# Performance work log

Hardware: AMD Instinct MI355X
Metric: run time of the kernel (lower is better)

## Reference

```python
import jax, jax.numpy as jnp
import numpy as np

HIDDEN = 2048
NUM_HEADS = 16
HEAD_DIM = HIDDEN // NUM_HEADS  # 128
ROPE_BASE = 10000.0


def setup_inputs() -> dict:
    key = jax.random.key(0)
    ks = jax.random.split(key, 5)
    B, T, C = 2, 2048, HIDDEN
    scale = 1.0 / np.sqrt(C)
    x = jax.random.normal(ks[0], (B, T, C), dtype=jnp.float32)
    Wq = jax.random.normal(ks[1], (C, C), dtype=jnp.float32) * scale
    Wk = jax.random.normal(ks[2], (C, C), dtype=jnp.float32) * scale
    Wv = jax.random.normal(ks[3], (C, C), dtype=jnp.float32) * scale
    Wo = jax.random.normal(ks[4], (C, C), dtype=jnp.float32) * scale
    return {"x": x, "Wq": Wq, "Wk": Wk, "Wv": Wv, "Wo": Wo}


def _rope_cos_sin(T, dtype):
    # inv_freq: [D/2]; emb: [T, D] = cat(freqs, freqs)
    inv_freq = 1.0 / (ROPE_BASE ** (jnp.arange(0, HEAD_DIM, 2, dtype=jnp.float32) / HEAD_DIM))
    t = jnp.arange(T, dtype=jnp.float32)
    freqs = t[:, None] * inv_freq[None, :]          # [T, D/2]
    emb = jnp.concatenate([freqs, freqs], axis=-1)  # [T, D]
    # broadcast shape [1, T, 1, D] to match q/k [B, T, H, D]
    return jnp.cos(emb)[None, :, None, :].astype(dtype), jnp.sin(emb)[None, :, None, :].astype(dtype)


def _rotate_half(u):
    u1, u2 = jnp.split(u, 2, axis=-1)
    return jnp.concatenate([-u2, u1], axis=-1)


def reference(x, Wq, Wk, Wv, Wo):
    B, T, C = x.shape
    H, D = NUM_HEADS, HEAD_DIM
    # QKV projections (torch Linear: x @ W.T). Weights here stored as [C, C] so use x @ W.
    q = (x @ Wq).reshape(B, T, H, D)
    k = (x @ Wk).reshape(B, T, H, D)
    v = (x @ Wv).reshape(B, T, H, D)
    cos, sin = _rope_cos_sin(T, x.dtype)
    q = q * cos + _rotate_half(q) * sin
    k = k * cos + _rotate_half(k) * sin
    # causal SDPA: scores [B, H, T, T]
    scale = 1.0 / jnp.sqrt(jnp.asarray(D, dtype=x.dtype))
    scores = jnp.einsum('bqhd,bkhd->bhqk', q, k) * scale
    causal = jnp.tril(jnp.ones((T, T), dtype=bool))
    scores = jnp.where(causal[None, None, :, :], scores, jnp.asarray(-jnp.inf, dtype=scores.dtype))
    attn = jax.nn.softmax(scores, axis=-1)
    out = jnp.einsum('bhqk,bkhd->bqhd', attn, v).reshape(B, T, C)
    return out @ Wo
```

## Files before the change

### kernel.cpp

```cpp
#include <hip/hip_runtime.h>
#include <hip/hip_bf16.h>

#define C_DIM 2048
#define NHEAD 16
#define HD 128
#define BB 2
#define TT 2048
#define MM (BB * TT)
#define NQT 32
#define N3 (3 * C_DIM)

typedef short short4v __attribute__((ext_vector_type(4)));
typedef short short8v __attribute__((ext_vector_type(8)));
typedef __bf16 bf16x4 __attribute__((ext_vector_type(4)));
typedef __bf16 bf16x8 __attribute__((ext_vector_type(8)));
typedef float f32x4 __attribute__((ext_vector_type(4)));

#define AS1 __attribute__((address_space(1)))
#define AS3 __attribute__((address_space(3)))

#define VMCNT(n) asm volatile("s_waitcnt vmcnt(" #n ")" ::: "memory")

__device__ __forceinline__ void load_lds16(const void* g, void* l) {
  __builtin_amdgcn_global_load_lds((const AS1 void*)g, (AS3 void*)l, 16, 0, 0);
}

__device__ __forceinline__ short f2bf(float f) {
  union { float f; unsigned u; } v; v.f = f;
  unsigned u = v.u;
  u += 0x7FFFu + ((u >> 16) & 1u);
  return (short)(u >> 16);
}
__device__ __forceinline__ float bf2f(short s) {
  union { unsigned u; float f; } v;
  v.u = ((unsigned)(unsigned short)s) << 16;
  return v.f;
}

__device__ __forceinline__ float exp2_fast(float x) {
  float r;
  asm("v_exp_f32 %0, %1" : "=v"(r) : "v"(x));
  return r;
}

__global__ __launch_bounds__(256) void cvt_x(const float* __restrict__ in,
                                             short* __restrict__ out, int n4) {
  int i = blockIdx.x * 256 + threadIdx.x;
  int stride = gridDim.x * 256;
  for (int idx = i; idx < n4; idx += stride) {
    float4 f = ((const float4*)in)[idx];
    short4v o;
    o[0] = f2bf(f.x); o[1] = f2bf(f.y); o[2] = f2bf(f.z); o[3] = f2bf(f.w);
    ((short4v*)out)[idx] = o;
  }
}

__global__ __launch_bounds__(256) void cvt_w_t(const float* __restrict__ W,
                                               short* __restrict__ Wt) {
  __shared__ float tile[32][33];
  int bx = blockIdx.x;
  int by = blockIdx.y;
  int lx = threadIdx.x & 31;
  int ly = threadIdx.x >> 5;
#pragma unroll
  for (int j = 0; j < 4; ++j) {
    int r = by * 32 + ly + j * 8;
    tile[ly + j * 8][lx] = W[(size_t)r * C_DIM + bx * 32 + lx];
  }
  __syncthreads();
#pragma unroll
  for (int j = 0; j < 4; ++j) {
    int n = bx * 32 + ly + j * 8;
    Wt[(size_t)n * C_DIM + by * 32 + lx] = f2bf(tile[lx][ly + j * 8]);
  }
}

__global__ __launch_bounds__(256) void rope_tab(float2* __restrict__ tab) {
  int idx = blockIdx.x * 256 + threadIdx.x;
  int t = idx >> 6, d = idx & 63;
  float inv = expf(-9.210340371976184f * (float)d * (1.0f / 64.0f));
  float a = (float)t * inv;
  tab[idx] = make_float2(cosf(a), sinf(a));
}

template <bool F32OUT>
__global__ __launch_bounds__(256, 2) void gemm8p(const short* __restrict__ A,
                                                 const short* __restrict__ Bt,
                                                 void* __restrict__ Cout,
                                                 int M, int N, int K, int NBN) {
  __shared__ short sA[2][128 * 64];
  __shared__ short sB[2][128 * 64];
  const int tid = threadIdx.x;
  const int lane = tid & 63;
  const int w = tid >> 6;
  const int wm = w >> 1, wn = w & 1;
  const int r = lane & 15, g = lane >> 4;

  const int wg = blockIdx.x;
  const int mb = wg / NBN, nb = wg % NBN;
  const int m0 = mb * 128, n0 = nb * 128;

  f32x4 acc[4][4] = {};

  auto stage = [&](int buf, int kt) {
#pragma unroll
    for (int j = 0; j < 4; ++j) {
      int p = j * 256 + tid;
      int row = p >> 3;
      int c16 = (p & 7) ^ (row & 7);
      load_lds16(A + (size_t)(m0 + row) * K + kt * 64 + c16 * 8,
                 &sA[buf][(j * 256 + w * 64) * 8]);
    }
#pragma unroll
    for (int j = 0; j < 4; ++j) {
      int p = j * 256 + tid;
      int row = p >> 3;
      int c16 = (p & 7) ^ (row & 7);
      load_lds16(Bt + (size_t)(n0 + row) * K + kt * 64 + c16 * 8,
                 &sB[buf][(j * 256 + w * 64) * 8]);
    }
  };

  auto compute = [&](int buf) {
#pragma unroll
    for (int kk = 0; kk < 2; ++kk) {
      bf16x8 af[4], bv[4];
#pragma unroll
      for (int m = 0; m < 4; ++m) {
        int row = wm * 64 + m * 16 + r;
        af[m] = *(const bf16x8*)((const char*)&sA[buf][0] + row * 128 +
                                 (((kk * 4 + g) ^ (row & 7)) << 4));
      }
#pragma unroll
      for (int n = 0; n < 4; ++n) {
        int row = wn * 64 + n * 16 + r;
        bv[n] = *(const bf16x8*)((const char*)&sB[buf][0] + row * 128 +
                                 (((kk * 4 + g) ^ (row & 7)) << 4));
      }
      __builtin_amdgcn_s_setprio(1);
#pragma unroll
      for (int m = 0; m < 4; ++m)
#pragma unroll
        for (int n = 0; n < 4; ++n)
          acc[m][n] = __builtin_amdgcn_mfma_f32_16x16x32_bf16(af[m], bv[n], acc[m][n], 0, 0, 0);
      __builtin_amdgcn_s_setprio(0);
    }
  };

  const int NT = K >> 6;
  stage(0, 0);
  stage(1, 1);
  VMCNT(8);
  __builtin_amdgcn_s_barrier();

  for (int t = 0; t < NT; ++t) {
    const int cur = t & 1;
    compute(cur);
    if (t + 1 < NT) {
      asm volatile("" ::: "memory");
      __builtin_amdgcn_s_barrier();
      if (t + 2 < NT) {
        stage(cur, t + 2);
        VMCNT(8);
      } else {
        VMCNT(0);
      }
      asm volatile("" ::: "memory");
      __builtin_amdgcn_s_barrier();
    }
  }

#pragma unroll
  for (int m = 0; m < 4; ++m)
#pragma unroll
    for (int n = 0; n < 4; ++n)
#pragma unroll
      for (int q = 0; q < 4; ++q) {
        int row = m0 + wm * 64 + m * 16 + g * 4 + q;
        int col = n0 + wn * 64 + n * 16 + r;
        size_t off = (size_t)row * N + col;
        if constexpr (F32OUT) ((float*)Cout)[off] = acc[m][n][q];
        else ((short*)Cout)[off] = f2bf(acc[m][n][q]);
      }
}

__global__ __launch_bounds__(256) void rope_qk(const short* __restrict__ qkv,
                                               const float2* __restrict__ tab,
                                               short* __restrict__ Qr,
                                               short* __restrict__ Kr) {
  const short* src = qkv + (blockIdx.y ? C_DIM : 0);
  short* dst = blockIdx.y ? Kr : Qr;
  const float qs = blockIdx.y ? 1.0f : 0.12751744f;
  int rid = blockIdx.x * 4 + (threadIdx.x >> 6);
  int lane = threadIdx.x & 63;
  int t = rid & (TT - 1);
  int bh = rid >> 11;
  int b = bh >> 4, h = bh & 15;
  const short* in = src + ((size_t)(b * TT + t)) * N3 + h * HD;
  float f0 = bf2f(in[lane]);
  float f1 = bf2f(in[lane + 64]);
  float2 cs = tab[t * 64 + lane];
  dst[(size_t)rid * HD + lane]      = f2bf((f0 * cs.x - f1 * cs.y) * qs);
  dst[(size_t)rid * HD + lane + 64] = f2bf((f1 * cs.x + f0 * cs.y) * qs);
}

__global__ __launch_bounds__(256) void v_tr(const short* __restrict__ qkv,
                                            short* __restrict__ Vt) {
  __shared__ short tl[64][132];
  int bh = blockIdx.y, b = bh >> 4, h = bh & 15;
  int t0 = blockIdx.x * 64;
  int tid = threadIdx.x;
  const short* vsrc = qkv + 2 * C_DIM;
#pragma unroll
  for (int i = 0; i < 4; ++i) {
    int c = i * 256 + tid;
    int row = c >> 4, cc = c & 15;
    short8v v = *(const short8v*)(vsrc + ((size_t)(b * TT + t0 + row)) * N3 + h * HD + cc * 8);
#pragma unroll
    for (int j = 0; j < 8; ++j) tl[row][cc * 8 + j] = v[j];
  }
  __syncthreads();
  int d = tid >> 1, half = tid & 1;
#pragma unroll
  for (int u = 0; u < 4; ++u) {
    short8v ov;
#pragma unroll
    for (int j = 0; j < 8; ++j) ov[j] = tl[half * 32 + u * 8 + j][d];
    *(short8v*)(Vt + ((size_t)bh * HD + d) * TT + t0 + half * 32 + u * 8) = ov;
  }
}

__global__ __launch_bounds__(256) void attn_dual(const short* __restrict__ Qr,
                                                 const short* __restrict__ Kr,
                                                 const short* __restrict__ Vt,
                                                 short* __restrict__ AO) {
  const int qa = blockIdx.x;
  const int qb = NQT - 1 - qa;
  const int bh = blockIdx.y;
  const int b = bh >> 4, h = bh & 15;
  const int tid = threadIdx.x;
  const int lane = tid & 63;
  const int w = tid >> 6;
  const int r = lane & 15, g = lane >> 4;

  __shared__ short sK[64 * 128];
  __shared__ short sV[128 * 64];
  __shared__ short sPa[4][16 * 72];
  __shared__ short sPb[4][16 * 72];

  auto loadQ = [&](bf16x8* qf, int q0) {
    const short* qbp = Qr + ((size_t)bh * TT + q0 + w * 16 + r) * HD + g * 8;
#pragma unroll
    for (int s = 0; s < 4; ++s) qf[s] = *(const bf16x8*)(qbp + s * 32);
  };

  bf16x8 qfA[4], qfB[4];
  loadQ(qfA, qa * 64);
  loadQ(qfB, qb * 64);

  f32x4 oA[8] = {}, oB[8] = {};
  float mA = -1e30f, mB = -1e30f;
  float lA = 0.f, lB = 0.f;

  short8v kreg[4], vreg[4];
  auto stage_load = [&](int kt) {
#pragma unroll
    for (int i = 0; i < 4; ++i) {
      int c = i * 256 + tid;
      kreg[i] = *(const short8v*)(Kr + ((size_t)bh * TT + kt * 64 + (c >> 4)) * HD + (c & 15) * 8);
    }
#pragma unroll
    for (int i = 0; i < 4; ++i) {
      int c = i * 256 + tid;
      vreg[i] = *(const short8v*)(Vt + ((size_t)bh * HD + (c >> 3)) * TT + kt * 64 + (c & 7) * 8);
    }
  };
  auto stage_write = [&]() {
#pragma unroll
    for (int i = 0; i < 4; ++i) {
      int c = i * 256 + tid;
      int row = c >> 4, cc = c & 15;
      int addr = (row * 256 + cc * 16) ^ ((row & 7) << 4);
      *(short8v*)((char*)sK + addr) = kreg[i];
    }
#pragma unroll
    for (int i = 0; i < 4; ++i) {
      int c = i * 256 + tid;
      int row = c >> 3, cc = c & 7;
      int addr = (row * 128 + cc * 16) ^ ((row & 7) << 4);
      *(short8v*)((char*)sV + addr) = vreg[i];
    }
  };

  auto process = [&](const bf16x8* qf, f32x4* o, float& m, float& l, bool diag,
                     short* pw) {
    f32x4 sacc[4] = {};
    __builtin_amdgcn_s_setprio(1);
#pragma unroll
    for (int nf = 0; nf < 4; ++nf) {
#pragma unroll
      for (int ss = 0; ss < 4; ++ss) {
        int krow = nf * 16 + r;
        int addr = (krow * 256 + (ss * 32 + g * 8) * 2) ^ ((krow & 7) << 4);
        bf16x8 kf = *(const bf16x8*)((char*)sK + addr);
        sacc[nf] = __builtin_amdgcn_mfma_f32_16x16x32_bf16(kf, qf[ss], sacc[nf], 0, 0, 0);
      }
    }
    __builtin_amdgcn_s_setprio(0);

    if (diag) {
#pragma unroll
      for (int nf = 0; nf < 4; ++nf)
#pragma unroll
        for (int q = 0; q < 4; ++q)
          if (nf * 16 + g * 4 + q > w * 16 + r) sacc[nf][q] = -1e30f;
    }

    float p01 = fmaxf(fmaxf(sacc[0][0], sacc[0][1]), fmaxf(sacc[0][2], sacc[0][3]));
    float p23 = fmaxf(fmaxf(sacc[1][0], sacc[1][1]), fmaxf(sacc[1][2], sacc[1][3]));
    float p45 = fmaxf(fmaxf(sacc[2][0], sacc[2][1]), fmaxf(sacc[2][2], sacc[2][3]));
    float p67 = fmaxf(fmaxf(sacc[3][0], sacc[3][1]), fmaxf(sacc[3][2], sacc[3][3]));
    float pmax = fmaxf(fmaxf(p01, p23), fmaxf(p45, p67));
    pmax = fmaxf(pmax, __shfl_xor(pmax, 16, 64));
    pmax = fmaxf(pmax, __shfl_xor(pmax, 32, 64));

    if (!__all(pmax - m <= 8.0f)) {
      float mnew = fmaxf(m, pmax);
      float alpha = exp2_fast(m - mnew);
      m = mnew;
      l *= alpha;
#pragma unroll
      for (int q = 0; q < 4; ++q) {
        float aq = __shfl(alpha, (g * 4 + q) | (lane & 48), 64);
#pragma unroll
        for (int nf2 = 0; nf2 < 8; ++nf2) o[nf2][q] *= aq;
      }
    }

    float s16 = 0.f;
#pragma unroll
    for (int nf = 0; nf < 4; ++nf) {
      f32x4 pe;
#pragma unroll
      for (int q = 0; q < 4; ++q) pe[q] = exp2_fast(sacc[nf][q] - m);
      s16 += (pe[0] + pe[1]) + (pe[2] + pe[3]);
      *(bf16x4*)(pw + r * 72 + nf * 16 + g * 4) = __builtin_convertvector(pe, bf16x4);
    }
    float rs = s16;
    rs += __shfl_xor(rs, 16, 64);
    rs += __shfl_xor(rs, 32, 64);
    l += rs;

    __builtin_amdgcn_s_setprio(1);
#pragma unroll
    for (int s2 = 0; s2 < 2; ++s2) {
      bf16x8 pa = *(const bf16x8*)(pw + r * 72 + s2 * 32 + g * 8);
#pragma unroll
      for (int nf2 = 0; nf2 < 8; ++nf2) {
        int drow = nf2 * 16 + r;
        int addr = (drow * 128 + (s2 * 32 + g * 8) * 2) ^ ((drow & 7) << 4);
        bf16x8 vb = *(const bf16x8*)((char*)sV + addr);
        o[nf2] = __builtin_amdgcn_mfma_f32_16x16x32_bf16(pa, vb, o[nf2], 0, 0, 0);
      }
    }
    __builtin_amdgcn_s_setprio(0);
  };

  stage_load(0);
  stage_write();
  __syncthreads();

  for (int kt = 0; kt <= qb; ++kt) {
    if (kt < qb) stage_load(kt + 1);

    process(qfB, oB, mB, lB, kt == qb, &sPb[w][0]);
    if (kt <= qa) process(qfA, oA, mA, lA, kt == qa, &sPa[w][0]);

    __syncthreads();
    if (kt < qb) {
      stage_write();
      __syncthreads();
    }
  }

  auto writeO = [&](f32x4* o, float l, int q0) {
    float linv = 1.0f / l;
    float lrow[4];
#pragma unroll
    for (int q = 0; q < 4; ++q)
      lrow[q] = __shfl(linv, (g * 4 + q) | (lane & 48), 64);
#pragma unroll
    for (int nf2 = 0; nf2 < 8; ++nf2)
#pragma unroll
      for (int q = 0; q < 4; ++q) {
        int t = q0 + w * 16 + g * 4 + q;
        int cc = h * HD + nf2 * 16 + r;
        AO[((size_t)b * TT + t) * C_DIM + cc] = f2bf(o[nf2][q] * lrow[q]);
      }
  };
  writeO(oA, lA, qa * 64);
  writeO(oB, lB, qb * 64);
}

extern "C" void kernel_launch(void* const* d_in, const int* in_sizes, int n_in,
                              void* d_out, int out_size, void* d_ws, size_t ws_size,
                              hipStream_t stream) {
  const float* x  = (const float*)d_in[0];
  const float* Wq = (const float*)d_in[1];
  const float* Wk = (const float*)d_in[2];
  const float* Wv = (const float*)d_in[3];
  const float* Wo = (const float*)d_in[4];

  char* ws = (char*)d_ws;
  size_t off = 0;
  auto take = [&](size_t bytes) {
    char* p = ws + off;
    off += (bytes + 255) & ~(size_t)255;
    return p;
  };
  const size_t xe = (size_t)MM * C_DIM;
  const size_t we = (size_t)C_DIM * C_DIM;
  short* xb   = (short*)take(xe * 2);
  short* wqkv = (short*)take(3 * we * 2);
  short* wot  = (short*)take(we * 2);
  short* qkv  = (short*)take(3 * xe * 2);
  short* Qr   = (short*)take(xe * 2);
  short* Kr   = (short*)take(xe * 2);
  short* Vtr  = (short*)take(xe * 2);
  float2* tab = (float2*)take((size_t)TT * 64 * sizeof(float2));
  short* AO   = qkv;

  cvt_x<<<2048, 256, 0, stream>>>(x, xb, (int)(xe / 4));
  cvt_w_t<<<dim3(64, 64), 256, 0, stream>>>(Wq, wqkv);
  cvt_w_t<<<dim3(64, 64), 256, 0, stream>>>(Wk, wqkv + we);
  cvt_w_t<<<dim3(64, 64), 256, 0, stream>>>(Wv, wqkv + 2 * we);
  cvt_w_t<<<dim3(64, 64), 256, 0, stream>>>(Wo, wot);
  rope_tab<<<(TT * 64) / 256, 256, 0, stream>>>(tab);

  gemm8p<false><<<1536, 256, 0, stream>>>(xb, wqkv, qkv, MM, N3, C_DIM, N3 / 128);

  rope_qk<<<dim3(16384, 2), 256, 0, stream>>>(qkv, tab, Qr, Kr);
  v_tr<<<dim3(32, 32), 256, 0, stream>>>(qkv, Vtr);

  attn_dual<<<dim3(16, 32), 256, 0, stream>>>(Qr, Kr, Vtr, AO);

  gemm8p<true><<<512, 256, 0, stream>>>(AO, wot, d_out, MM, C_DIM, C_DIM, C_DIM / 128);
}
```

Measured before the change: 329.7 us.

## Split dual-tile attention into one query tile per block with longest-first ordering

The attention kernel now gives each block a single 64-row query tile instead of a pair of complementary tiles, launching 1024 blocks. Block order puts the longest causal tiles first and interleaves short ones to balance load across CUs. Launch bounds request 4 blocks per CU, and the P scratch buffer uses an XOR-swizzled layout instead of padding. The aim is more occupancy and better latency hiding, at the cost of each K/V tile feeding only one query tile, which doubles K/V loads and adds register pressure from the launch bound.

```diff
diff --git a/kernel.cpp b/kernel.cpp
--- a/kernel.cpp
+++ b/kernel.cpp
@@ -230,13 +230,13 @@
   }
 }
 
-__global__ __launch_bounds__(256) void attn_dual(const short* __restrict__ Qr,
-                                                 const short* __restrict__ Kr,
-                                                 const short* __restrict__ Vt,
-                                                 short* __restrict__ AO) {
-  const int qa = blockIdx.x;
-  const int qb = NQT - 1 - qa;
-  const int bh = blockIdx.y;
+__global__ __launch_bounds__(256, 4) void attn_one(const short* __restrict__ Qr,
+                                                   const short* __restrict__ Kr,
+                                                   const short* __restrict__ Vt,
+                                                   short* __restrict__ AO) {
+  const int bx = blockIdx.x;
+  const int j = bx >> 5, bh = bx & 31;
+  const int qt = (j & 1) ? (j >> 1) : (NQT - 1 - (j >> 1));
   const int b = bh >> 4, h = bh & 15;
   const int tid = threadIdx.x;
   const int lane = tid & 63;
@@ -245,22 +245,17 @@
 
   __shared__ short sK[64 * 128];
   __shared__ short sV[128 * 64];
-  __shared__ short sPa[4][16 * 72];
-  __shared__ short sPb[4][16 * 72];
-
-  auto loadQ = [&](bf16x8* qf, int q0) {
-    const short* qbp = Qr + ((size_t)bh * TT + q0 + w * 16 + r) * HD + g * 8;
+  __shared__ short sP[4][16 * 64];
+
+  bf16x8 qf[4];
+  {
+    const short* qbp = Qr + ((size_t)bh * TT + qt * 64 + w * 16 + r) * HD + g * 8;
 #pragma unroll
     for (int s = 0; s < 4; ++s) qf[s] = *(const bf16x8*)(qbp + s * 32);
-  };
-
-  bf16x8 qfA[4], qfB[4];
-  loadQ(qfA, qa * 64);
-  loadQ(qfB, qb * 64);
-
-  f32x4 oA[8] = {}, oB[8] = {};
-  float mA = -1e30f, mB = -1e30f;
-  float lA = 0.f, lB = 0.f;
+  }
+
+  f32x4 o[8] = {};
+  float m = -1e30f, l = 0.f;
 
   short8v kreg[4], vreg[4];
   auto stage_load = [&](int kt) {
@@ -292,8 +287,15 @@
     }
   };
 
-  auto process = [&](const bf16x8* qf, f32x4* o, float& m, float& l, bool diag,
-                     short* pw) {
+  char* pw = (char*)&sP[w][0];
+
+  stage_load(0);
+  stage_write();
+  __syncthreads();
+
+  for (int kt = 0; kt <= qt; ++kt) {
+    if (kt < qt) stage_load(kt + 1);
+
     f32x4 sacc[4] = {};
     __builtin_amdgcn_s_setprio(1);
 #pragma unroll
@@ -308,7 +310,7 @@
     }
     __builtin_amdgcn_s_setprio(0);
 
-    if (diag) {
+    if (kt == qt) {
 #pragma unroll
       for (int nf = 0; nf < 4; ++nf)
 #pragma unroll
@@ -344,7 +346,8 @@
 #pragma unroll
       for (int q = 0; q < 4; ++q) pe[q] = exp2_fast(sacc[nf][q] - m);
       s16 += (pe[0] + pe[1]) + (pe[2] + pe[3]);
-      *(bf16x4*)(pw + r * 72 + nf * 16 + g * 4) = __builtin_convertvector(pe, bf16x4);
+      int addr = (r * 128 + nf * 32 + g * 8) ^ ((r & 7) << 4);
+      *(bf16x4*)(pw + addr) = __builtin_convertvector(pe, bf16x4);
     }
     float rs = s16;
     rs += __shfl_xor(rs, 16, 64);
@@ -354,7 +357,8 @@
     __builtin_amdgcn_s_setprio(1);
 #pragma unroll
     for (int s2 = 0; s2 < 2; ++s2) {
-      bf16x8 pa = *(const bf16x8*)(pw + r * 72 + s2 * 32 + g * 8);
+      int paddr = (r * 128 + s2 * 64 + g * 16) ^ ((r & 7) << 4);
+      bf16x8 pa = *(const bf16x8*)(pw + paddr);
 #pragma unroll
       for (int nf2 = 0; nf2 < 8; ++nf2) {
         int drow = nf2 * 16 + r;
@@ -364,42 +368,27 @@
       }
     }
     __builtin_amdgcn_s_setprio(0);
-  };
-
-  stage_load(0);
-  stage_write();
-  __syncthreads();
-
-  for (int kt = 0; kt <= qb; ++kt) {
-    if (kt < qb) stage_load(kt + 1);
-
-    process(qfB, oB, mB, lB, kt == qb, &sPb[w][0]);
-    if (kt <= qa) process(qfA, oA, mA, lA, kt == qa, &sPa[w][0]);
 
     __syncthreads();
-    if (kt < qb) {
+    if (kt < qt) {
       stage_write();
       __syncthreads();
     }
   }
 
-  auto writeO = [&](f32x4* o, float l, int q0) {
-    float linv = 1.0f / l;
-    float lrow[4];
-#pragma unroll
-    for (int q = 0; q < 4; ++q)
-      lrow[q] = __shfl(linv, (g * 4 + q) | (lane & 48), 64);
-#pragma unroll
-    for (int nf2 = 0; nf2 < 8; ++nf2)
-#pragma unroll
-      for (int q = 0; q < 4; ++q) {
-        int t = q0 + w * 16 + g * 4 + q;
-        int cc = h * HD + nf2 * 16 + r;
-        AO[((size_t)b * TT + t) * C_DIM + cc] = f2bf(o[nf2][q] * lrow[q]);
-      }
-  };
-  writeO(oA, lA, qa * 64);
-  writeO(oB, lB, qb * 64);
+  float linv = 1.0f / l;
+  float lrow[4];
+#pragma unroll
+  for (int q = 0; q < 4; ++q)
+    lrow[q] = __shfl(linv, (g * 4 + q) | (lane & 48), 64);
+#pragma unroll
+  for (int nf2 = 0; nf2 < 8; ++nf2)
+#pragma unroll
+    for (int q = 0; q < 4; ++q) {
+      int t = qt * 64 + w * 16 + g * 4 + q;
+      int cc = h * HD + nf2 * 16 + r;
+      AO[((size_t)b * TT + t) * C_DIM + cc] = f2bf(o[nf2][q] * lrow[q]);
+    }
 }
 
 extern "C" void kernel_launch(void* const* d_in, const int* in_sizes, int n_in,
@@ -442,7 +431,7 @@
   rope_qk<<<dim3(16384, 2), 256, 0, stream>>>(qkv, tab, Qr, Kr);
   v_tr<<<dim3(32, 32), 256, 0, stream>>>(qkv, Vtr);
 
-  attn_dual<<<dim3(16, 32), 256, 0, stream>>>(Qr, Kr, Vtr, AO);
+  attn_one<<<1024, 256, 0, stream>>>(Qr, Kr, Vtr, AO);
 
   gemm8p<true><<<512, 256, 0, stream>>>(AO, wot, d_out, MM, C_DIM, C_DIM, C_DIM / 128);
 }
```

Result: slower. 470.0 us (+42.6%).
